# Kernel tuning notes

Hardware: AMD Instinct MI355X
Metric: run time of the kernel (lower is better)

## Reference

```python
import jax, jax.numpy as jnp
import numpy as np

N_NODES = 100000
BASE_DIM = 128
E1 = 500000
E2 = 250000
N_TYPES = 4


def setup_inputs() -> dict:
    key = jax.random.key(0)
    ks = jax.random.split(key, 9)
    x = jax.random.normal(ks[0], (N_NODES, BASE_DIM), dtype=jnp.float32)
    # per-edge-type dense transforms (shape-1: d->d, shape-2: 2d->d)
    W1 = jax.random.normal(ks[1], (N_TYPES, BASE_DIM, BASE_DIM), dtype=jnp.float32) * 0.05
    W2 = jax.random.normal(ks[2], (N_TYPES, 2 * BASE_DIM, BASE_DIM), dtype=jnp.float32) * 0.05
    src1 = jax.random.randint(ks[3], (E1,), 0, N_NODES, dtype=jnp.int32)
    tgt1 = jax.random.randint(ks[4], (E1,), 0, N_NODES, dtype=jnp.int32)
    type1 = jax.random.randint(ks[5], (E1,), 0, N_TYPES, dtype=jnp.int32)
    src2 = jax.random.randint(ks[6], (2 * E2,), 0, N_NODES, dtype=jnp.int32)
    tgt2 = jax.random.randint(ks[7], (E2,), 0, N_NODES, dtype=jnp.int32)
    type2 = jax.random.randint(ks[8], (E2,), 0, N_TYPES, dtype=jnp.int32)
    return {"x": x, "W1": W1, "W2": W2, "src1": src1, "tgt1": tgt1,
            "type1": type1, "src2": src2, "tgt2": tgt2, "type2": type2}


def _gather_transform_scatter(x, W, src, tgt, etype, arity, n_nodes):
    # gather `arity` source nodes per hyperedge and concat features: (E, arity*d)
    d = x.shape[1]
    concat = x[src].reshape(-1, arity * d)
    # per-edge-type dense transform; small loop over fixed #types, masked accumulate
    acc = jnp.zeros((concat.shape[0], d), dtype=x.dtype)
    for t in range(W.shape[0]):
        acc = acc + jnp.where((etype == t)[:, None], concat @ W[t], 0.0)
    # scatter-add messages to target nodes
    return jax.ops.segment_sum(acc, tgt, num_segments=n_nodes)


def reference(x, W1, W2, src1, tgt1, type1, src2, tgt2, type2):
    n = x.shape[0]
    out = x
    out = out + _gather_transform_scatter(x, W1, src1, tgt1, type1, 1, n)
    out = out + _gather_transform_scatter(x, W2, src2, tgt2, type2, 2, n)
    return out
```

## Files before the change

kernel.cpp:

```cpp
#include <hip/hip_runtime.h>
#include <hip/hip_bf16.h>

#define D 128
#define EPB 32
#define NB 256

typedef __attribute__((ext_vector_type(8))) short bf16x8;
typedef __attribute__((ext_vector_type(4))) float f32x4;

__device__ inline unsigned short f2bf(float f) {
    union { float f; unsigned int u; } v;
    v.f = f;
    unsigned int u = v.u;
    unsigned int r = u + 0x7fffu + ((u >> 16) & 1u);
    return (unsigned short)(r >> 16);
}

__global__ __launch_bounds__(256) void copy_kernel(float* __restrict__ out,
                                                   const float* __restrict__ x,
                                                   int n_elems) {
    int n4 = n_elems >> 2;
    const float4* src = (const float4*)x;
    float4* dst = (float4*)out;
    for (int i = blockIdx.x * blockDim.x + threadIdx.x; i < n4;
         i += gridDim.x * blockDim.x)
        dst[i] = src[i];
}

__global__ __launch_bounds__(256) void conv_w(const float* __restrict__ W,
                                              unsigned short* __restrict__ Wt,
                                              int K) {
    __shared__ float tile[32][33];
    int k0 = blockIdx.x * 32, c0 = blockIdx.y * 32, t = blockIdx.z;
    int tr = threadIdx.x >> 5, tc = threadIdx.x & 31;
#pragma unroll
    for (int m = 0; m < 4; m++)
        tile[m * 8 + tr][tc] = W[((size_t)t * K + k0 + m * 8 + tr) * D + c0 + tc];
    __syncthreads();
#pragma unroll
    for (int m = 0; m < 4; m++)
        Wt[((size_t)t * D + c0 + m * 8 + tr) * K + k0 + tc] = f2bf(tile[tc][m * 8 + tr]);
}

__global__ __launch_bounds__(256) void hist_types(const int* __restrict__ type,
                                                  int n, int* __restrict__ hist) {
    __shared__ int h[4];
    if (threadIdx.x < 4) h[threadIdx.x] = 0;
    __syncthreads();
    for (int i = blockIdx.x * 256 + threadIdx.x; i < n; i += NB * 256)
        atomicAdd(&h[type[i]], 1);
    __syncthreads();
    if (threadIdx.x < 4) hist[blockIdx.x * 4 + threadIdx.x] = h[threadIdx.x];
}

__global__ void scan_offsets(int* __restrict__ meta,
                             const int* __restrict__ hist1, int* __restrict__ off1,
                             const int* __restrict__ hist2, int* __restrict__ off2) {
    int t = threadIdx.x;
    if (t < 4) {
        int s = 0;
        for (int b = 0; b < NB; b++) s += hist1[b * 4 + t];
        meta[t] = s;
    } else if (t < 8) {
        int tt = t - 4, s = 0;
        for (int b = 0; b < NB; b++) s += hist2[b * 4 + tt];
        meta[4 + tt] = s;
    }
    __syncthreads();
    if (t == 0) {
        int p = 0;
        for (int k = 0; k < 4; k++) {
            meta[8 + k] = p;
            p += ((meta[k] + EPB - 1) / EPB) * EPB;
        }
        meta[12] = p;
        p = 0;
        for (int k = 0; k < 4; k++) {
            meta[13 + k] = p;
            p += ((meta[4 + k] + EPB - 1) / EPB) * EPB;
        }
        meta[17] = p;
    }
    __syncthreads();
    if (t < 4) {
        int p = meta[8 + t];
        for (int b = 0; b < NB; b++) { off1[b * 4 + t] = p; p += hist1[b * 4 + t]; }
    } else if (t < 8) {
        int tt = t - 4;
        int p = meta[13 + tt];
        for (int b = 0; b < NB; b++) { off2[b * 4 + tt] = p; p += hist2[b * 4 + tt]; }
    }
}

__global__ __launch_bounds__(256) void write_sorted(const int* __restrict__ type,
                                                    int n,
                                                    const int* __restrict__ off,
                                                    int* __restrict__ sorted) {
    __shared__ int loff[4];
    if (threadIdx.x < 4) loff[threadIdx.x] = off[blockIdx.x * 4 + threadIdx.x];
    __syncthreads();
    for (int i = blockIdx.x * 256 + threadIdx.x; i < n; i += NB * 256) {
        int t = type[i];
        int pos = atomicAdd(&loff[t], 1);
        sorted[pos] = i;
    }
}


__global__ __launch_bounds__(256) void edge1_mfma(
    const float* __restrict__ x, const unsigned short* __restrict__ Wt1,
    const int* __restrict__ src, const int* __restrict__ tgt,
    const int* __restrict__ sorted, const int* __restrict__ meta,
    float* __restrict__ out) {
    __shared__ uint4 As4[512];
    __shared__ int s_tgt[EPB];
    __shared__ int s_src[EPB];
    char* As = (char*)As4;

    int tid = threadIdx.x;
    int g0 = blockIdx.x * EPB;
    const int* pb = meta + 8;
    int t = 0;
#pragma unroll
    for (int k = 1; k < 4; k++)
        if (g0 >= pb[k]) t = k;
    const unsigned short* __restrict__ W = Wt1 + (size_t)t * D * D;

    if (tid < EPB) {
        int eid = sorted[g0 + tid];
        int sv = -1, tv = -1;
        if (eid >= 0) { sv = src[eid]; tv = tgt[eid]; }
        s_src[tid] = sv;
        s_tgt[tid] = tv;
    }
    __syncthreads();

    {
        int r = tid >> 3, u0 = tid & 7;
        int sv = s_src[r];
        const float4* srow = (const float4*)(x + (size_t)sv * D);
#pragma unroll
        for (int q = 0; q < 4; q++) {
            int u = u0 + 8 * q;
            float4 v = make_float4(0.f, 0.f, 0.f, 0.f);
            if (sv >= 0) v = srow[u];
            uint2 p;
            p.x = (unsigned)f2bf(v.x) | ((unsigned)f2bf(v.y) << 16);
            p.y = (unsigned)f2bf(v.z) | ((unsigned)f2bf(v.w) << 16);
            int byte = ((((u >> 1) * 16) ^ ((r & 7) << 4)) + (u & 1) * 8);
            *(uint2*)(As + r * 256 + byte) = p;
        }
    }
    __syncthreads();

    int wave = tid >> 6, lane = tid & 63;
    int c0 = wave * 32;
    int lrow = lane & 15, lgrp = lane >> 4;

    bf16x8 b[2][4];
#pragma unroll
    for (int fc = 0; fc < 2; fc++)
#pragma unroll
        for (int kk = 0; kk < 4; kk++)
            b[fc][kk] = *(const bf16x8*)(W + (size_t)(c0 + fc * 16 + lrow) * D +
                                         kk * 32 + lgrp * 8);

    f32x4 acc[2][2];
#pragma unroll
    for (int i = 0; i < 2; i++)
#pragma unroll
        for (int j = 0; j < 2; j++) acc[i][j] = (f32x4){0.f, 0.f, 0.f, 0.f};

#pragma unroll
    for (int kk = 0; kk < 4; kk++) {
        bf16x8 a0, a1;
        {
            int r = lrow;
            a0 = *(const bf16x8*)(As + r * 256 +
                                  ((kk * 64 + lgrp * 16) ^ ((r & 7) << 4)));
        }
        {
            int r = 16 + lrow;
            a1 = *(const bf16x8*)(As + r * 256 +
                                  ((kk * 64 + lgrp * 16) ^ ((r & 7) << 4)));
        }
        acc[0][0] = __builtin_amdgcn_mfma_f32_16x16x32_bf16(a0, b[0][kk], acc[0][0], 0, 0, 0);
        acc[1][0] = __builtin_amdgcn_mfma_f32_16x16x32_bf16(a1, b[0][kk], acc[1][0], 0, 0, 0);
        acc[0][1] = __builtin_amdgcn_mfma_f32_16x16x32_bf16(a0, b[1][kk], acc[0][1], 0, 0, 0);
        acc[1][1] = __builtin_amdgcn_mfma_f32_16x16x32_bf16(a1, b[1][kk], acc[1][1], 0, 0, 0);
    }

#pragma unroll
    for (int fr = 0; fr < 2; fr++)
#pragma unroll
        for (int reg = 0; reg < 4; reg++) {
            int erow = fr * 16 + lgrp * 4 + reg;
            int tv = s_tgt[erow];
            if (tv >= 0) {
#pragma unroll
                for (int fc = 0; fc < 2; fc++)
                    atomicAdd(&out[(size_t)tv * D + c0 + fc * 16 + lrow],
                              acc[fr][fc][reg]);
            }
        }
}

__global__ __launch_bounds__(256) void edge2_mfma(
    const float* __restrict__ x, const unsigned short* __restrict__ Wt2,
    const int* __restrict__ src2, const int* __restrict__ tgt,
    const int* __restrict__ sorted, const int* __restrict__ meta,
    float* __restrict__ out) {
    __shared__ uint4 As4[1024];
    __shared__ int s_tgt[EPB];
    __shared__ int s_srcA[EPB];
    __shared__ int s_srcB[EPB];
    char* As = (char*)As4;

    int tid = threadIdx.x;
    int g0 = blockIdx.x * EPB;
    const int* pb = meta + 13;
    int t = 0;
#pragma unroll
    for (int k = 1; k < 4; k++)
        if (g0 >= pb[k]) t = k;
    const unsigned short* __restrict__ W = Wt2 + (size_t)t * D * 2 * D;

    if (tid < EPB) {
        int eid = sorted[g0 + tid];
        int sa = -1, sb = -1, tv = -1;
        if (eid >= 0) { sa = src2[2 * eid]; sb = src2[2 * eid + 1]; tv = tgt[eid]; }
        s_srcA[tid] = sa;
        s_srcB[tid] = sb;
        s_tgt[tid] = tv;
    }
    __syncthreads();

    {
        int r = tid >> 3, u0 = tid & 7;
        int sa = s_srcA[r], sb = s_srcB[r];
        const float4* rowA = (const float4*)(x + (size_t)sa * D);
        const float4* rowB = (const float4*)(x + (size_t)sb * D);
#pragma unroll
        for (int q = 0; q < 8; q++) {
            int u = u0 + 8 * q;
            float4 v = make_float4(0.f, 0.f, 0.f, 0.f);
            if (sa >= 0) v = (u < 32) ? rowA[u] : rowB[u - 32];
            uint2 p;
            p.x = (unsigned)f2bf(v.x) | ((unsigned)f2bf(v.y) << 16);
            p.y = (unsigned)f2bf(v.z) | ((unsigned)f2bf(v.w) << 16);
            int byte = ((((u >> 1) * 16) ^ ((r & 7) << 4)) + (u & 1) * 8);
            *(uint2*)(As + r * 512 + byte) = p;
        }
    }
    __syncthreads();

    int wave = tid >> 6, lane = tid & 63;
    int c0 = wave * 32;
    int lrow = lane & 15, lgrp = lane >> 4;

    f32x4 acc[2][2];
#pragma unroll
    for (int i = 0; i < 2; i++)
#pragma unroll
        for (int j = 0; j < 2; j++) acc[i][j] = (f32x4){0.f, 0.f, 0.f, 0.f};

#pragma unroll
    for (int kk = 0; kk < 8; kk++) {
        bf16x8 b0 = *(const bf16x8*)(W + (size_t)(c0 + lrow) * 2 * D + kk * 32 + lgrp * 8);
        bf16x8 b1 = *(const bf16x8*)(W + (size_t)(c0 + 16 + lrow) * 2 * D + kk * 32 + lgrp * 8);
        bf16x8 a0, a1;
        {
            int r = lrow;
            a0 = *(const bf16x8*)(As + r * 512 +
                                  ((kk * 64 + lgrp * 16) ^ ((r & 7) << 4)));
        }
        {
            int r = 16 + lrow;
            a1 = *(const bf16x8*)(As + r * 512 +
                                  ((kk * 64 + lgrp * 16) ^ ((r & 7) << 4)));
        }
        acc[0][0] = __builtin_amdgcn_mfma_f32_16x16x32_bf16(a0, b0, acc[0][0], 0, 0, 0);
        acc[1][0] = __builtin_amdgcn_mfma_f32_16x16x32_bf16(a1, b0, acc[1][0], 0, 0, 0);
        acc[0][1] = __builtin_amdgcn_mfma_f32_16x16x32_bf16(a0, b1, acc[0][1], 0, 0, 0);
        acc[1][1] = __builtin_amdgcn_mfma_f32_16x16x32_bf16(a1, b1, acc[1][1], 0, 0, 0);
    }

#pragma unroll
    for (int fr = 0; fr < 2; fr++)
#pragma unroll
        for (int reg = 0; reg < 4; reg++) {
            int erow = fr * 16 + lgrp * 4 + reg;
            int tv = s_tgt[erow];
            if (tv >= 0) {
#pragma unroll
                for (int fc = 0; fc < 2; fc++)
                    atomicAdd(&out[(size_t)tv * D + c0 + fc * 16 + lrow],
                              acc[fr][fc][reg]);
            }
        }
}

__global__ __launch_bounds__(256) void e1_simple(
    const float* __restrict__ x, const float* __restrict__ W1,
    const int* __restrict__ src, const int* __restrict__ tgt,
    const int* __restrict__ type, float* __restrict__ out, int n) {
    int lane = threadIdx.x & 63;
    int wid = (blockIdx.x * blockDim.x + threadIdx.x) >> 6;
    int nw = (gridDim.x * blockDim.x) >> 6;
    for (int e = wid; e < n; e += nw) {
        const float* W = W1 + (size_t)type[e] * D * D;
        const float* xr = x + (size_t)src[e] * D;
        float a0 = 0.f, a1 = 0.f;
        for (int i = 0; i < D; i++) {
            float xv = xr[i];
            a0 = fmaf(xv, W[i * D + lane], a0);
            a1 = fmaf(xv, W[i * D + 64 + lane], a1);
        }
        atomicAdd(&out[(size_t)tgt[e] * D + lane], a0);
        atomicAdd(&out[(size_t)tgt[e] * D + 64 + lane], a1);
    }
}

__global__ __launch_bounds__(256) void e2_simple(
    const float* __restrict__ x, const float* __restrict__ W2,
    const int* __restrict__ src2, const int* __restrict__ tgt,
    const int* __restrict__ type, float* __restrict__ out, int n) {
    int lane = threadIdx.x & 63;
    int wid = (blockIdx.x * blockDim.x + threadIdx.x) >> 6;
    int nw = (gridDim.x * blockDim.x) >> 6;
    for (int e = wid; e < n; e += nw) {
        const float* W = W2 + (size_t)type[e] * 2 * D * D;
        const float* xrA = x + (size_t)src2[2 * e] * D;
        const float* xrB = x + (size_t)src2[2 * e + 1] * D;
        float a0 = 0.f, a1 = 0.f;
        for (int i = 0; i < 2 * D; i++) {
            float xv = (i < D) ? xrA[i] : xrB[i - D];
            a0 = fmaf(xv, W[i * D + lane], a0);
            a1 = fmaf(xv, W[i * D + 64 + lane], a1);
        }
        atomicAdd(&out[(size_t)tgt[e] * D + lane], a0);
        atomicAdd(&out[(size_t)tgt[e] * D + 64 + lane], a1);
    }
}

extern "C" void kernel_launch(void* const* d_in, const int* in_sizes, int n_in,
                              void* d_out, int out_size, void* d_ws, size_t ws_size,
                              hipStream_t stream) {
    const float* x = (const float*)d_in[0];
    const float* W1 = (const float*)d_in[1];
    const float* W2 = (const float*)d_in[2];
    const int* src1 = (const int*)d_in[3];
    const int* tgt1 = (const int*)d_in[4];
    const int* type1 = (const int*)d_in[5];
    const int* src2 = (const int*)d_in[6];
    const int* tgt2 = (const int*)d_in[7];
    const int* type2 = (const int*)d_in[8];
    float* out = (float*)d_out;

    int n_nodes = in_sizes[0] / D;
    int E1c = in_sizes[3];
    int E2c = in_sizes[7];

    copy_kernel<<<2048, 256, 0, stream>>>(out, x, n_nodes * D);

    int grid1 = (E1c + 4 * (EPB - 1) + EPB - 1) / EPB;
    int grid2 = (E2c + 4 * (EPB - 1) + EPB - 1) / EPB;
    int cap1 = grid1 * EPB;
    int cap2 = grid2 * EPB;

    size_t ints_head = 32 + (size_t)4 * NB * 4;
    size_t base = ints_head * 4 + (size_t)4 * (cap1 + cap2);
    base = (base + 255) & ~(size_t)255;
    size_t w1_elems = (size_t)4 * D * D;
    size_t w2_elems = (size_t)4 * D * 2 * D;
    size_t need = base + (w1_elems + w2_elems) * 2;

    if (ws_size >= need) {
        int* meta = (int*)d_ws;
        int* hist1 = meta + 32;
        int* off1 = hist1 + NB * 4;
        int* hist2 = off1 + NB * 4;
        int* off2 = hist2 + NB * 4;
        int* sorted1 = off2 + NB * 4;
        int* sorted2 = sorted1 + cap1;
        unsigned short* wt1 = (unsigned short*)((char*)d_ws + base);
        unsigned short* wt2 = wt1 + w1_elems;

        hipMemsetAsync(sorted1, 0xFF, (size_t)4 * (cap1 + cap2), stream);

        conv_w<<<dim3(4, 4, 4), 256, 0, stream>>>(W1, wt1, D);
        conv_w<<<dim3(8, 4, 4), 256, 0, stream>>>(W2, wt2, 2 * D);

        hist_types<<<NB, 256, 0, stream>>>(type1, E1c, hist1);
        hist_types<<<NB, 256, 0, stream>>>(type2, E2c, hist2);
        scan_offsets<<<1, 64, 0, stream>>>(meta, hist1, off1, hist2, off2);
        write_sorted<<<NB, 256, 0, stream>>>(type1, E1c, off1, sorted1);
        write_sorted<<<NB, 256, 0, stream>>>(type2, E2c, off2, sorted2);

        edge1_mfma<<<grid1, 256, 0, stream>>>(x, wt1, src1, tgt1, sorted1, meta, out);
        edge2_mfma<<<grid2, 256, 0, stream>>>(x, wt2, src2, tgt2, sorted2, meta, out);
    } else {
        e1_simple<<<2048, 256, 0, stream>>>(x, W1, src1, tgt1, type1, out, E1c);
        e2_simple<<<2048, 256, 0, stream>>>(x, W2, src2, tgt2, type2, out, E2c);
    }
}
```

Before: 401.0 us.

## Replace atomic scatter with CSR-grouped bf16 message buffer and per-node reduction

Builds a per-target-node CSR (counts via atomics, a single-block scan, and a per-edge slot) and has the MFMA edge kernels write bf16 messages into that slot rather than atomically adding fp32 into the output. A finalize kernel then reads x plus each node's contiguous messages and writes the output once, which removes the initial copy and the float atomics. In exchange it adds a large message buffer (about 192 MB of bf16 traffic written and read), several extra kernels including a serial-ish 1024-thread scan over 100k nodes, and bf16 rounding of messages before summation. The path needs a large workspace and falls back to the old atomic path otherwise.

New measurement: 496.7 us. 1.24x slower.

```diff
diff --git a/kernel.cpp b/kernel.cpp
--- a/kernel.cpp
+++ b/kernel.cpp
@@ -14,6 +14,11 @@
     unsigned int u = v.u;
     unsigned int r = u + 0x7fffu + ((u >> 16) & 1u);
     return (unsigned short)(r >> 16);
+}
+__device__ inline float bf2f(unsigned short b) {
+    union { unsigned int u; float f; } v;
+    v.u = ((unsigned int)b) << 16;
+    return v.f;
 }
 
 __global__ __launch_bounds__(256) void copy_kernel(float* __restrict__ out,
@@ -106,6 +111,252 @@
     }
 }
 
+__global__ __launch_bounds__(256) void assign_rel(const int* __restrict__ tgt, int n,
+                                                  int* __restrict__ cnt,
+                                                  int* __restrict__ pos) {
+    for (int i = blockIdx.x * blockDim.x + threadIdx.x; i < n;
+         i += gridDim.x * blockDim.x)
+        pos[i] = atomicAdd(&cnt[tgt[i]], 1);
+}
+
+__global__ __launch_bounds__(1024) void scan_count(const int* __restrict__ cnt, int n,
+                                                   int* __restrict__ base) {
+    __shared__ int part[1024];
+    int t = threadIdx.x;
+    int chunk = (n + 1023) >> 10;
+    int lo = min(t * chunk, n), hi = min(lo + chunk, n);
+    int s = 0;
+    for (int i = lo; i < hi; i++) s += cnt[i];
+    part[t] = s;
+    __syncthreads();
+    for (int off = 1; off < 1024; off <<= 1) {
+        int v = part[t];
+        if (t >= off) v += part[t - off];
+        __syncthreads();
+        part[t] = v;
+        __syncthreads();
+    }
+    int run = (t > 0) ? part[t - 1] : 0;
+    for (int i = lo; i < hi; i++) { base[i] = run; run += cnt[i]; }
+    if (lo < n && hi == n) base[n] = run;
+}
+
+
+__global__ __launch_bounds__(256) void edge1_msg(
+    const float* __restrict__ x, const unsigned short* __restrict__ Wt1,
+    const int* __restrict__ src, const int* __restrict__ tgt,
+    const int* __restrict__ sorted, const int* __restrict__ meta,
+    const int* __restrict__ basep, const int* __restrict__ pos,
+    unsigned short* __restrict__ msg) {
+    __shared__ uint4 As4[512];
+    __shared__ int s_mrow[EPB];
+    __shared__ int s_src[EPB];
+    char* As = (char*)As4;
+
+    int tid = threadIdx.x;
+    int g0 = blockIdx.x * EPB;
+    const int* pb = meta + 8;
+    int t = 0;
+#pragma unroll
+    for (int k = 1; k < 4; k++)
+        if (g0 >= pb[k]) t = k;
+    const unsigned short* __restrict__ W = Wt1 + (size_t)t * D * D;
+
+    if (tid < EPB) {
+        int eid = sorted[g0 + tid];
+        int sv = -1, mr = -1;
+        if (eid >= 0) { sv = src[eid]; mr = basep[tgt[eid]] + pos[eid]; }
+        s_src[tid] = sv;
+        s_mrow[tid] = mr;
+    }
+    __syncthreads();
+
+    {
+        int r = tid >> 3, u0 = tid & 7;
+        int sv = s_src[r];
+        const float4* srow = (const float4*)(x + (size_t)sv * D);
+#pragma unroll
+        for (int q = 0; q < 4; q++) {
+            int u = u0 + 8 * q;
+            float4 v = make_float4(0.f, 0.f, 0.f, 0.f);
+            if (sv >= 0) v = srow[u];
+            uint2 p;
+            p.x = (unsigned)f2bf(v.x) | ((unsigned)f2bf(v.y) << 16);
+            p.y = (unsigned)f2bf(v.z) | ((unsigned)f2bf(v.w) << 16);
+            int byte = ((((u >> 1) * 16) ^ ((r & 7) << 4)) + (u & 1) * 8);
+            *(uint2*)(As + r * 256 + byte) = p;
+        }
+    }
+    __syncthreads();
+
+    int wave = tid >> 6, lane = tid & 63;
+    int c0 = wave * 32;
+    int lrow = lane & 15, lgrp = lane >> 4;
+
+    bf16x8 b[2][4];
+#pragma unroll
+    for (int fc = 0; fc < 2; fc++)
+#pragma unroll
+        for (int kk = 0; kk < 4; kk++)
+            b[fc][kk] = *(const bf16x8*)(W + (size_t)(c0 + fc * 16 + lrow) * D +
+                                         kk * 32 + lgrp * 8);
+
+    f32x4 acc[2][2];
+#pragma unroll
+    for (int i = 0; i < 2; i++)
+#pragma unroll
+        for (int j = 0; j < 2; j++) acc[i][j] = (f32x4){0.f, 0.f, 0.f, 0.f};
+
+#pragma unroll
+    for (int kk = 0; kk < 4; kk++) {
+        bf16x8 a0, a1;
+        {
+            int r = lrow;
+            a0 = *(const bf16x8*)(As + r * 256 +
+                                  ((kk * 64 + lgrp * 16) ^ ((r & 7) << 4)));
+        }
+        {
+            int r = 16 + lrow;
+            a1 = *(const bf16x8*)(As + r * 256 +
+                                  ((kk * 64 + lgrp * 16) ^ ((r & 7) << 4)));
+        }
+        acc[0][0] = __builtin_amdgcn_mfma_f32_16x16x32_bf16(a0, b[0][kk], acc[0][0], 0, 0, 0);
+        acc[1][0] = __builtin_amdgcn_mfma_f32_16x16x32_bf16(a1, b[0][kk], acc[1][0], 0, 0, 0);
+        acc[0][1] = __builtin_amdgcn_mfma_f32_16x16x32_bf16(a0, b[1][kk], acc[0][1], 0, 0, 0);
+        acc[1][1] = __builtin_amdgcn_mfma_f32_16x16x32_bf16(a1, b[1][kk], acc[1][1], 0, 0, 0);
+    }
+
+#pragma unroll
+    for (int fr = 0; fr < 2; fr++)
+#pragma unroll
+        for (int reg = 0; reg < 4; reg++) {
+            int erow = fr * 16 + lgrp * 4 + reg;
+            int mr = s_mrow[erow];
+            if (mr >= 0) {
+#pragma unroll
+                for (int fc = 0; fc < 2; fc++)
+                    msg[(size_t)mr * D + c0 + fc * 16 + lrow] =
+                        f2bf(acc[fr][fc][reg]);
+            }
+        }
+}
+
+__global__ __launch_bounds__(256) void edge2_msg(
+    const float* __restrict__ x, const unsigned short* __restrict__ Wt2,
+    const int* __restrict__ src2, const int* __restrict__ tgt,
+    const int* __restrict__ sorted, const int* __restrict__ meta,
+    const int* __restrict__ basep, const int* __restrict__ pos,
+    unsigned short* __restrict__ msg) {
+    __shared__ uint4 As4[1024];
+    __shared__ int s_mrow[EPB];
+    __shared__ int s_srcA[EPB];
+    __shared__ int s_srcB[EPB];
+    char* As = (char*)As4;
+
+    int tid = threadIdx.x;
+    int g0 = blockIdx.x * EPB;
+    const int* pb = meta + 13;
+    int t = 0;
+#pragma unroll
+    for (int k = 1; k < 4; k++)
+        if (g0 >= pb[k]) t = k;
+    const unsigned short* __restrict__ W = Wt2 + (size_t)t * D * 2 * D;
+
+    if (tid < EPB) {
+        int eid = sorted[g0 + tid];
+        int sa = -1, sb = -1, mr = -1;
+        if (eid >= 0) {
+            sa = src2[2 * eid];
+            sb = src2[2 * eid + 1];
+            mr = basep[tgt[eid]] + pos[eid];
+        }
+        s_srcA[tid] = sa;
+        s_srcB[tid] = sb;
+        s_mrow[tid] = mr;
+    }
+    __syncthreads();
+
+    {
+        int r = tid >> 3, u0 = tid & 7;
+        int sa = s_srcA[r], sb = s_srcB[r];
+        const float4* rowA = (const float4*)(x + (size_t)sa * D);
+        const float4* rowB = (const float4*)(x + (size_t)sb * D);
+#pragma unroll
+        for (int q = 0; q < 8; q++) {
+            int u = u0 + 8 * q;
+            float4 v = make_float4(0.f, 0.f, 0.f, 0.f);
+            if (sa >= 0) v = (u < 32) ? rowA[u] : rowB[u - 32];
+            uint2 p;
+            p.x = (unsigned)f2bf(v.x) | ((unsigned)f2bf(v.y) << 16);
+            p.y = (unsigned)f2bf(v.z) | ((unsigned)f2bf(v.w) << 16);
+            int byte = ((((u >> 1) * 16) ^ ((r & 7) << 4)) + (u & 1) * 8);
+            *(uint2*)(As + r * 512 + byte) = p;
+        }
+    }
+    __syncthreads();
+
+    int wave = tid >> 6, lane = tid & 63;
+    int c0 = wave * 32;
+    int lrow = lane & 15, lgrp = lane >> 4;
+
+    f32x4 acc[2][2];
+#pragma unroll
+    for (int i = 0; i < 2; i++)
+#pragma unroll
+        for (int j = 0; j < 2; j++) acc[i][j] = (f32x4){0.f, 0.f, 0.f, 0.f};
+
+#pragma unroll
+    for (int kk = 0; kk < 8; kk++) {
+        bf16x8 b0 = *(const bf16x8*)(W + (size_t)(c0 + lrow) * 2 * D + kk * 32 + lgrp * 8);
+        bf16x8 b1 = *(const bf16x8*)(W + (size_t)(c0 + 16 + lrow) * 2 * D + kk * 32 + lgrp * 8);
+        bf16x8 a0, a1;
+        {
+            int r = lrow;
+            a0 = *(const bf16x8*)(As + r * 512 +
+                                  ((kk * 64 + lgrp * 16) ^ ((r & 7) << 4)));
+        }
+        {
+            int r = 16 + lrow;
+            a1 = *(const bf16x8*)(As + r * 512 +
+                                  ((kk * 64 + lgrp * 16) ^ ((r & 7) << 4)));
+        }
+        acc[0][0] = __builtin_amdgcn_mfma_f32_16x16x32_bf16(a0, b0, acc[0][0], 0, 0, 0);
+        acc[1][0] = __builtin_amdgcn_mfma_f32_16x16x32_bf16(a1, b0, acc[1][0], 0, 0, 0);
+        acc[0][1] = __builtin_amdgcn_mfma_f32_16x16x32_bf16(a0, b1, acc[0][1], 0, 0, 0);
+        acc[1][1] = __builtin_amdgcn_mfma_f32_16x16x32_bf16(a1, b1, acc[1][1], 0, 0, 0);
+    }
+
+#pragma unroll
+    for (int fr = 0; fr < 2; fr++)
+#pragma unroll
+        for (int reg = 0; reg < 4; reg++) {
+            int erow = fr * 16 + lgrp * 4 + reg;
+            int mr = s_mrow[erow];
+            if (mr >= 0) {
+#pragma unroll
+                for (int fc = 0; fc < 2; fc++)
+                    msg[(size_t)mr * D + c0 + fc * 16 + lrow] =
+                        f2bf(acc[fr][fc][reg]);
+            }
+        }
+}
+
+__global__ __launch_bounds__(256) void finalize(
+    const float* __restrict__ x, const unsigned short* __restrict__ msg,
+    const int* __restrict__ basep, float* __restrict__ out, int nn) {
+    int wib = threadIdx.x >> 6, lane = threadIdx.x & 63;
+    for (int v = blockIdx.x * 4 + wib; v < nn; v += gridDim.x * 4) {
+        int b0 = basep[v], b1 = basep[v + 1];
+        float2 xv = *(const float2*)(x + (size_t)v * D + lane * 2);
+        float a0 = xv.x, a1 = xv.y;
+        for (int i = b0; i < b1; i++) {
+            unsigned u = *(const unsigned*)(msg + (size_t)i * D + lane * 2);
+            a0 += bf2f((unsigned short)(u & 0xffff));
+            a1 += bf2f((unsigned short)(u >> 16));
+        }
+        *(float2*)(out + (size_t)v * D + lane * 2) = make_float2(a0, a1);
+    }
+}
 
 __global__ __launch_bounds__(256) void edge1_mfma(
     const float* __restrict__ x, const unsigned short* __restrict__ Wt1,
@@ -134,7 +385,6 @@
         s_tgt[tid] = tv;
     }
     __syncthreads();
-
     {
         int r = tid >> 3, u0 = tid & 7;
         int sv = s_src[r];
@@ -176,13 +426,11 @@
         bf16x8 a0, a1;
         {
             int r = lrow;
-            a0 = *(const bf16x8*)(As + r * 256 +
-                                  ((kk * 64 + lgrp * 16) ^ ((r & 7) << 4)));
+            a0 = *(const bf16x8*)(As + r * 256 + ((kk * 64 + lgrp * 16) ^ ((r & 7) << 4)));
         }
         {
             int r = 16 + lrow;
-            a1 = *(const bf16x8*)(As + r * 256 +
-                                  ((kk * 64 + lgrp * 16) ^ ((r & 7) << 4)));
+            a1 = *(const bf16x8*)(As + r * 256 + ((kk * 64 + lgrp * 16) ^ ((r & 7) << 4)));
         }
         acc[0][0] = __builtin_amdgcn_mfma_f32_16x16x32_bf16(a0, b[0][kk], acc[0][0], 0, 0, 0);
         acc[1][0] = __builtin_amdgcn_mfma_f32_16x16x32_bf16(a1, b[0][kk], acc[1][0], 0, 0, 0);
@@ -234,7 +482,6 @@
         s_tgt[tid] = tv;
     }
     __syncthreads();
-
     {
         int r = tid >> 3, u0 = tid & 7;
         int sa = s_srcA[r], sb = s_srcB[r];
@@ -271,13 +518,11 @@
         bf16x8 a0, a1;
         {
             int r = lrow;
-            a0 = *(const bf16x8*)(As + r * 512 +
-                                  ((kk * 64 + lgrp * 16) ^ ((r & 7) << 4)));
+            a0 = *(const bf16x8*)(As + r * 512 + ((kk * 64 + lgrp * 16) ^ ((r & 7) << 4)));
         }
         {
             int r = 16 + lrow;
-            a1 = *(const bf16x8*)(As + r * 512 +
-                                  ((kk * 64 + lgrp * 16) ^ ((r & 7) << 4)));
+            a1 = *(const bf16x8*)(As + r * 512 + ((kk * 64 + lgrp * 16) ^ ((r & 7) << 4)));
         }
         acc[0][0] = __builtin_amdgcn_mfma_f32_16x16x32_bf16(a0, b0, acc[0][0], 0, 0, 0);
         acc[1][0] = __builtin_amdgcn_mfma_f32_16x16x32_bf16(a1, b0, acc[1][0], 0, 0, 0);
@@ -357,36 +602,60 @@
     const int* type2 = (const int*)d_in[8];
     float* out = (float*)d_out;
 
-    int n_nodes = in_sizes[0] / D;
+    int nn = in_sizes[0] / D;
     int E1c = in_sizes[3];
     int E2c = in_sizes[7];
-
-    copy_kernel<<<2048, 256, 0, stream>>>(out, x, n_nodes * D);
 
     int grid1 = (E1c + 4 * (EPB - 1) + EPB - 1) / EPB;
     int grid2 = (E2c + 4 * (EPB - 1) + EPB - 1) / EPB;
     int cap1 = grid1 * EPB;
     int cap2 = grid2 * EPB;
 
-    size_t ints_head = 32 + (size_t)4 * NB * 4;
-    size_t base = ints_head * 4 + (size_t)4 * (cap1 + cap2);
-    base = (base + 255) & ~(size_t)255;
+    size_t o_meta = 0;
+    size_t o_hist1 = o_meta + 32;
+    size_t o_off1 = o_hist1 + (size_t)NB * 4;
+    size_t o_hist2 = o_off1 + (size_t)NB * 4;
+    size_t o_off2 = o_hist2 + (size_t)NB * 4;
+    size_t o_sorted1 = o_off2 + (size_t)NB * 4;
+    size_t o_sorted2 = o_sorted1 + cap1;
+    size_t o_pos1 = o_sorted2 + cap2;
+    size_t o_pos2 = o_pos1 + E1c;
+    size_t o_cnt = o_pos2 + E2c;
+    size_t o_base = o_cnt + nn;
+    size_t ints_full = o_base + nn + 1;
+    size_t ints_r3 = o_pos1;
+
     size_t w1_elems = (size_t)4 * D * D;
     size_t w2_elems = (size_t)4 * D * 2 * D;
-    size_t need = base + (w1_elems + w2_elems) * 2;
-
-    if (ws_size >= need) {
-        int* meta = (int*)d_ws;
-        int* hist1 = meta + 32;
-        int* off1 = hist1 + NB * 4;
-        int* hist2 = off1 + NB * 4;
-        int* off2 = hist2 + NB * 4;
-        int* sorted1 = off2 + NB * 4;
-        int* sorted2 = sorted1 + cap1;
-        unsigned short* wt1 = (unsigned short*)((char*)d_ws + base);
+
+    size_t wb_full = (ints_full * 4 + 255) & ~(size_t)255;
+    size_t wb_r3 = (ints_r3 * 4 + 255) & ~(size_t)255;
+    size_t wt_bytes = (w1_elems + w2_elems) * 2;
+
+    size_t msg_off = (wb_full + wt_bytes + 255) & ~(size_t)255;
+    size_t msg_bytes = (size_t)(E1c + E2c) * D * 2;
+    size_t need_full = msg_off + msg_bytes;
+    size_t need_r3 = wb_r3 + wt_bytes;
+
+    if (ws_size >= need_full) {
+        int* wsI = (int*)d_ws;
+        int* meta = wsI + o_meta;
+        int* hist1 = wsI + o_hist1;
+        int* off1 = wsI + o_off1;
+        int* hist2 = wsI + o_hist2;
+        int* off2 = wsI + o_off2;
+        int* sorted1 = wsI + o_sorted1;
+        int* sorted2 = wsI + o_sorted2;
+        int* pos1 = wsI + o_pos1;
+        int* pos2 = wsI + o_pos2;
+        int* cnt = wsI + o_cnt;
+        int* basep = wsI + o_base;
+        unsigned short* wt1 = (unsigned short*)((char*)d_ws + wb_full);
         unsigned short* wt2 = wt1 + w1_elems;
+        unsigned short* msg = (unsigned short*)((char*)d_ws + msg_off);
 
         hipMemsetAsync(sorted1, 0xFF, (size_t)4 * (cap1 + cap2), stream);
+        hipMemsetAsync(cnt, 0, (size_t)4 * nn, stream);
 
         conv_w<<<dim3(4, 4, 4), 256, 0, stream>>>(W1, wt1, D);
         conv_w<<<dim3(8, 4, 4), 256, 0, stream>>>(W2, wt2, 2 * D);
@@ -397,9 +666,44 @@
         write_sorted<<<NB, 256, 0, stream>>>(type1, E1c, off1, sorted1);
         write_sorted<<<NB, 256, 0, stream>>>(type2, E2c, off2, sorted2);
 
+        assign_rel<<<2048, 256, 0, stream>>>(tgt1, E1c, cnt, pos1);
+        assign_rel<<<2048, 256, 0, stream>>>(tgt2, E2c, cnt, pos2);
+        scan_count<<<1, 1024, 0, stream>>>(cnt, nn, basep);
+
+        edge1_msg<<<grid1, 256, 0, stream>>>(x, wt1, src1, tgt1, sorted1, meta,
+                                             basep, pos1, msg);
+        edge2_msg<<<grid2, 256, 0, stream>>>(x, wt2, src2, tgt2, sorted2, meta,
+                                             basep, pos2, msg);
+
+        finalize<<<(nn + 3) / 4, 256, 0, stream>>>(x, msg, basep, out, nn);
+    } else if (ws_size >= need_r3) {
+        int* wsI = (int*)d_ws;
+        int* meta = wsI + o_meta;
+        int* hist1 = wsI + o_hist1;
+        int* off1 = wsI + o_off1;
+        int* hist2 = wsI + o_hist2;
+        int* off2 = wsI + o_off2;
+        int* sorted1 = wsI + o_sorted1;
+        int* sorted2 = wsI + o_sorted2;
+        unsigned short* wt1 = (unsigned short*)((char*)d_ws + wb_r3);
+        unsigned short* wt2 = wt1 + w1_elems;
+
+        copy_kernel<<<2048, 256, 0, stream>>>(out, x, nn * D);
+        hipMemsetAsync(sorted1, 0xFF, (size_t)4 * (cap1 + cap2), stream);
+
+        conv_w<<<dim3(4, 4, 4), 256, 0, stream>>>(W1, wt1, D);
+        conv_w<<<dim3(8, 4, 4), 256, 0, stream>>>(W2, wt2, 2 * D);
+
+        hist_types<<<NB, 256, 0, stream>>>(type1, E1c, hist1);
+        hist_types<<<NB, 256, 0, stream>>>(type2, E2c, hist2);
+        scan_offsets<<<1, 64, 0, stream>>>(meta, hist1, off1, hist2, off2);
+        write_sorted<<<NB, 256, 0, stream>>>(type1, E1c, off1, sorted1);
+        write_sorted<<<NB, 256, 0, stream>>>(type2, E2c, off2, sorted2);
+
         edge1_mfma<<<grid1, 256, 0, stream>>>(x, wt1, src1, tgt1, sorted1, meta, out);
         edge2_mfma<<<grid2, 256, 0, stream>>>(x, wt2, src2, tgt2, sorted2, meta, out);
     } else {
+        copy_kernel<<<2048, 256, 0, stream>>>(out, x, nn * D);
         e1_simple<<<2048, 256, 0, stream>>>(x, W1, src1, tgt1, type1, out, E1c);
         e2_simple<<<2048, 256, 0, stream>>>(x, W2, src2, tgt2, type2, out, E2c);
     }
```
